# Performance work log

Measured on AMD Instinct MI355X. Metric: run time of the kernel, lower is better.

## Reference

```python
import jax, jax.numpy as jnp
import numpy as np

N = 10000
E = 320000
D_IN = 256
D_H = 256
D_OUT = 64
NEG_SLOPE = 0.2


def _segment_softmax(scores, seg, num_segments):
    # numerically stable softmax over variable-size neighborhoods
    m = jax.ops.segment_max(scores, seg, num_segments=num_segments)
    e = jnp.exp(scores - m[seg])
    s = jax.ops.segment_sum(e, seg, num_segments=num_segments)
    return e / s[seg]


def _gatv2_conv(x, src, dst, Wl, bl, Wr, br, att, bias):
    # PyG GATv2Conv, heads=1: lin_l on source, lin_r on target
    xl = x @ Wl + bl              # [N, C]
    xr = x @ Wr + br              # [N, C]
    xj = xl[src]                  # [E, C] source messages
    e = jax.nn.leaky_relu(xj + xr[dst], NEG_SLOPE)   # [E, C]
    score = e @ att               # [E]
    alpha = _segment_softmax(score, dst, N)          # [E]
    out = jax.ops.segment_sum(alpha[:, None] * xj, dst, num_segments=N)
    return out + bias


def setup_inputs() -> dict:
    key = jax.random.key(0)
    ks = jax.random.split(key, 16)
    s1 = 1.0 / np.sqrt(D_IN)
    s2 = 1.0 / np.sqrt(D_H)
    x = jax.random.normal(ks[0], (N, D_IN), dtype=jnp.float32)
    edge_index = jax.random.randint(ks[1], (2, E), 0, N, dtype=jnp.int64)
    return {
        "x": x,
        "W1l": jax.random.normal(ks[2], (D_IN, D_H), jnp.float32) * s1,
        "b1l": jnp.zeros((D_H,), jnp.float32),
        "W1r": jax.random.normal(ks[3], (D_IN, D_H), jnp.float32) * s1,
        "b1r": jnp.zeros((D_H,), jnp.float32),
        "att1": jax.random.normal(ks[4], (D_H,), jnp.float32) * s2,
        "bias1": jnp.zeros((D_H,), jnp.float32),
        "W2l": jax.random.normal(ks[5], (D_H, D_H), jnp.float32) * s2,
        "b2l": jnp.zeros((D_H,), jnp.float32),
        "W2r": jax.random.normal(ks[6], (D_H, D_H), jnp.float32) * s2,
        "b2r": jnp.zeros((D_H,), jnp.float32),
        "att2": jax.random.normal(ks[7], (D_H,), jnp.float32) * s2,
        "bias2": jnp.zeros((D_H,), jnp.float32),
        "Wout": jax.random.normal(ks[8], (D_H, D_OUT), jnp.float32) * s2,
        "bout": jnp.zeros((D_OUT,), jnp.float32),
        "edge_index": edge_index,
    }


def reference(x, W1l, b1l, W1r, b1r, att1, bias1,
              W2l, b2l, W2r, b2r, att2, bias2,
              Wout, bout, edge_index):
    # add self loops (PyG GATv2Conv default)
    loops = jnp.arange(N, dtype=edge_index.dtype)
    src = jnp.concatenate([edge_index[0], loops])
    dst = jnp.concatenate([edge_index[1], loops])

    h = _gatv2_conv(x, src, dst, W1l, b1l, W1r, b1r, att1, bias1)
    h = jax.nn.relu(h)            # norm=Identity, dropout inactive (eval)
    h = _gatv2_conv(h, src, dst, W2l, b2l, W2r, b2r, att2, bias2)
    h = jax.nn.relu(h)
    logits = h @ Wout + bout      # [N, D_OUT]
    return jax.nn.log_softmax(logits, axis=1)
```

## Files before the change

kernel.cpp:

```cpp
#include <hip/hip_runtime.h>
#include <hip/hip_bf16.h>
#include <math.h>

#define N_NODES 10000
#define N_EDGES 320000
#define TOT_E (N_EDGES + N_NODES)
#define D 256
#define DOUT 64
#define NEG_SLOPE 0.2f
#define MAXDEG 128

typedef __attribute__((ext_vector_type(8))) short bf16x8;
typedef __attribute__((ext_vector_type(4))) float f32x4;
typedef unsigned short ushort_t;

__device__ __forceinline__ unsigned short f2b_rne(float f) {
    unsigned int x = __float_as_uint(f);
    x += 0x7FFFu + ((x >> 16) & 1u);
    return (unsigned short)(x >> 16);
}
__device__ __forceinline__ float b2f(unsigned short h) {
    return __uint_as_float(((unsigned int)h) << 16);
}
__device__ __forceinline__ void bsplit(float v, unsigned short& hi, unsigned short& lo) {
    hi = f2b_rne(v);
    lo = f2b_rne(v - b2f(hi));
}

__device__ __forceinline__ bool detect_f32(const void* x) {
    const ushort_t* xb = (const ushort_t*)x;
    int lane = threadIdx.x & 63;
    int bad = 0;
    #pragma unroll
    for (int i = 0; i < 4; ++i) {
        float v = b2f(xb[2 * (lane + 64 * i)]);
        bad += !(fabsf(v) < 1e4f) ? 1 : 0;
    }
    #pragma unroll
    for (int o = 32; o > 0; o >>= 1) bad += __shfl_down(bad, o);
    return __shfl(bad, 0) > 8;
}
__device__ __forceinline__ bool detect_i64(const int* e32) {
    int lane = threadIdx.x & 63;
    int nz = (e32[2 * lane + 1] != 0) ? 1 : 0;
    #pragma unroll
    for (int o = 32; o > 0; o >>= 1) nz += __shfl_down(nz, o);
    return __shfl(nz, 0) == 0;
}

__global__ __launch_bounds__(256) void prep_kernel(
        const void* x, ushort_t* xh, ushort_t* xlo,
        const void* W1l, const void* W1r, const void* W2l, const void* W2r, const void* Wo,
        const void* v0, const void* v1, const void* v2, const void* v3,
        const void* v4, const void* v5, const void* v6, const void* v7, const void* v8,
        ushort_t* wt, float* vecf, int* counts) {
    bool f32s = detect_f32(x);
    int bid = blockIdx.x;
    int t = threadIdx.x;
    if (bid < 2500) {
        int i = bid * 1024 + t * 4;
        float v[4];
        if (f32s) {
            float4 f = *(const float4*)((const float*)x + i);
            v[0] = f.x; v[1] = f.y; v[2] = f.z; v[3] = f.w;
        } else {
            union { uint2 q; ushort_t u[4]; } r;
            r.q = *(const uint2*)((const ushort_t*)x + i);
            #pragma unroll
            for (int j = 0; j < 4; ++j) v[j] = b2f(r.u[j]);
        }
        union { uint2 q; ushort_t u[4]; } H, L;
        #pragma unroll
        for (int j = 0; j < 4; ++j) bsplit(v[j], H.u[j], L.u[j]);
        *(uint2*)(xh + i) = H.q;
        *(uint2*)(xlo + i) = L.q;
    } else if (bid < 3588) {
        int b = bid - 2500;
        const void* srcs5[5] = {W1l, W1r, W2l, W2r, Wo};
        int wid, n, ncols;
        if (b < 1024) { wid = b >> 8; n = b & 255; ncols = 256; }
        else          { wid = 4;      n = b - 1024; ncols = 64; }
        ushort_t* dh;
        ushort_t* dl;
        if (wid < 4) { dh = wt + (size_t)wid * 2 * 65536; dl = dh + 65536; }
        else         { dh = wt + (size_t)8 * 65536;       dl = dh + 16384; }
        float v = f32s ? ((const float*)srcs5[wid])[(size_t)t * ncols + n]
                       : b2f(((const ushort_t*)srcs5[wid])[(size_t)t * ncols + n]);
        unsigned short hi, lo;
        bsplit(v, hi, lo);
        dh[(size_t)n * 256 + t] = hi;
        dl[(size_t)n * 256 + t] = lo;
    } else if (bid < 3597) {
        int b = bid - 3588;
        const void* ps[9] = {v0, v1, v2, v3, v4, v5, v6, v7, v8};
        int n = (b == 8) ? DOUT : 256;
        if (t < n) {
            float v = f32s ? ((const float*)ps[b])[t] : b2f(((const ushort_t*)ps[b])[t]);
            vecf[b * 256 + t] = v;
        }
    } else {
        int idx = (bid - 3597) * 256 + t;
        if (idx < N_NODES) counts[idx] = 0;
    }
}

__device__ __forceinline__ int eload(const int* ei, bool is64, int idx) {
    int v = is64 ? ei[2 * (size_t)idx] : ei[idx];
    return ((unsigned)v < (unsigned)N_NODES) ? v : 0;
}

__global__ __launch_bounds__(256) void scatter_kernel(const int* __restrict__ ei,
                                                      int* __restrict__ counts,
                                                      int* __restrict__ srcs_pad) {
    bool is64 = detect_i64(ei);
    int id = blockIdx.x * 256 + threadIdx.x;
    if (id >= TOT_E) return;
    int src, dst;
    if (id < N_EDGES) { src = eload(ei, is64, id); dst = eload(ei, is64, N_EDGES + id); }
    else              { src = dst = id - N_EDGES; }
    int slot = atomicAdd(&counts[dst], 1);
    if (slot < MAXDEG) srcs_pad[dst * MAXDEG + slot] = src;
}

__global__ __launch_bounds__(256) void gemm_mfma_kernel(
        const ushort_t* __restrict__ Ahg, const ushort_t* __restrict__ Alg,
        const ushort_t* __restrict__ Wh0, const ushort_t* __restrict__ Wl0,
        const float* __restrict__ bias0, ushort_t* __restrict__ out0,
        const ushort_t* __restrict__ Wh1, const ushort_t* __restrict__ Wl1,
        const float* __restrict__ bias1, float* __restrict__ out1) {
    __shared__ bf16x8 Ah[4][64];
    __shared__ bf16x8 Al[4][64];
    __shared__ bf16x8 Bh[4][64];
    __shared__ bf16x8 Bl[4][64];
    int tid = threadIdx.x;
    int lane = tid & 63, wave = tid >> 6;
    int row0 = blockIdx.y * 64;
    int y = blockIdx.x;
    const ushort_t* Wh; const ushort_t* Wl; const float* bias;
    int col0;
    bool ob_bf16;
    if (y < 4) { Wh = Wh0; Wl = Wl0; bias = bias0; col0 = y * 64; ob_bf16 = true; }
    else       { Wh = Wh1; Wl = Wl1; bias = bias1; col0 = (y - 4) * 64; ob_bf16 = false; }
    int sm = tid >> 2;
    int skq = tid & 3;
    int sl = skq * 16 + (sm & 15);
    int sr = sm >> 4;

    f32x4 acc[4];
    #pragma unroll
    for (int c = 0; c < 4; ++c) acc[c] = (f32x4){0.f, 0.f, 0.f, 0.f};

    for (int k0 = 0; k0 < D; k0 += 32) {
        uint4 qah, qal;
        int grow = row0 + sm;
        if (grow < N_NODES) {
            size_t aoff = (size_t)grow * D + k0 + skq * 8;
            qah = *(const uint4*)(Ahg + aoff);
            qal = *(const uint4*)(Alg + aoff);
        } else {
            qah = (uint4){0, 0, 0, 0}; qal = (uint4){0, 0, 0, 0};
        }
        size_t boff = (size_t)(col0 + sm) * 256 + k0 + skq * 8;
        uint4 qbh = *(const uint4*)(Wh + boff);
        uint4 qbl = *(const uint4*)(Wl + boff);

        __syncthreads();
        *(uint4*)&Ah[sr][sl] = qah;
        *(uint4*)&Al[sr][sl] = qal;
        *(uint4*)&Bh[sr][sl] = qbh;
        *(uint4*)&Bl[sr][sl] = qbl;
        __syncthreads();

        bf16x8 a_h = Ah[wave][lane];
        bf16x8 a_l = Al[wave][lane];
        #pragma unroll
        for (int c = 0; c < 4; ++c) {
            bf16x8 b_h = Bh[c][lane];
            bf16x8 b_l = Bl[c][lane];
            acc[c] = __builtin_amdgcn_mfma_f32_16x16x32_bf16(a_h, b_l, acc[c], 0, 0, 0);
            acc[c] = __builtin_amdgcn_mfma_f32_16x16x32_bf16(a_l, b_h, acc[c], 0, 0, 0);
            acc[c] = __builtin_amdgcn_mfma_f32_16x16x32_bf16(a_h, b_h, acc[c], 0, 0, 0);
        }
    }
    int quad = lane >> 4;
    #pragma unroll
    for (int c = 0; c < 4; ++c) {
        int col = col0 + c * 16 + (lane & 15);
        float bv = bias[col];
        #pragma unroll
        for (int i = 0; i < 4; ++i) {
            int row = row0 + wave * 16 + quad * 4 + i;
            if (row < N_NODES) {
                float v = acc[c][i] + bv;
                if (ob_bf16) out0[(size_t)row * D + col] = f2b_rne(v);
                else         out1[(size_t)row * D + col] = v;
            }
        }
    }
}

__global__ __launch_bounds__(256) void conv_kernel(const ushort_t* __restrict__ xl,
                                                   const float* __restrict__ xr,
                                                   const float* __restrict__ att,
                                                   const float* __restrict__ bias,
                                                   const int* __restrict__ counts,
                                                   const int* __restrict__ srcs_pad,
                                                   ushort_t* __restrict__ hh,
                                                   ushort_t* __restrict__ hl) {
    __shared__ float xr_s[D];
    __shared__ float sc[MAXDEG];
    __shared__ int srcs_s[MAXDEG];
    int node = blockIdx.x;
    int t = threadIdx.x;
    int lane = t & 63, wave = t >> 6;
    int deg = counts[node];
    if (deg > MAXDEG) deg = MAXDEG;
    if (deg <= 0) {
        float o = fmaxf(bias[t], 0.f);
        unsigned short hi, lo; bsplit(o, hi, lo);
        hh[(size_t)node * D + t] = hi;
        hl[(size_t)node * D + t] = lo;
        return;
    }
    xr_s[t] = xr[(size_t)node * D + t];
    if (t < deg) srcs_s[t] = srcs_pad[node * MAXDEG + t];
    __syncthreads();

    int hw = t >> 5;
    int seg = t & 31;
    float xr8[8], att8[8];
    {
        float4 x0 = *(const float4*)&xr_s[seg * 8];
        float4 x1 = *(const float4*)&xr_s[seg * 8 + 4];
        float4 a0 = *(const float4*)(att + seg * 8);
        float4 a1 = *(const float4*)(att + seg * 8 + 4);
        xr8[0] = x0.x; xr8[1] = x0.y; xr8[2] = x0.z; xr8[3] = x0.w;
        xr8[4] = x1.x; xr8[5] = x1.y; xr8[6] = x1.z; xr8[7] = x1.w;
        att8[0] = a0.x; att8[1] = a0.y; att8[2] = a0.z; att8[3] = a0.w;
        att8[4] = a1.x; att8[5] = a1.y; att8[6] = a1.z; att8[7] = a1.w;
    }
    for (int e = hw; e < deg; e += 8) {
        int src = srcs_s[e];
        union { uint4 q; ushort_t u[8]; } r;
        r.q = *(const uint4*)(xl + (size_t)src * D + seg * 8);
        float p = 0.f;
        #pragma unroll
        for (int j = 0; j < 8; ++j) {
            float v = b2f(r.u[j]) + xr8[j];
            v = fmaxf(v, NEG_SLOPE * v);
            p += v * att8[j];
        }
        #pragma unroll
        for (int o = 16; o > 0; o >>= 1) p += __shfl_down(p, o, 32);
        if (seg == 0) sc[e] = isfinite(p) ? p : -1e30f;
    }
    __syncthreads();
    if (wave == 0) {
        float v0 = (lane < deg) ? sc[lane] : -INFINITY;
        float v1 = (lane + 64 < deg) ? sc[lane + 64] : -INFINITY;
        float mx = fmaxf(v0, v1);
        #pragma unroll
        for (int o = 32; o > 0; o >>= 1) mx = fmaxf(mx, __shfl_xor(mx, o));
        float e0 = (lane < deg) ? expf(v0 - mx) : 0.f;
        float e1 = (lane + 64 < deg) ? expf(v1 - mx) : 0.f;
        float s = e0 + e1;
        #pragma unroll
        for (int o = 32; o > 0; o >>= 1) s += __shfl_xor(s, o);
        float inv = 1.f / s;
        if (lane < deg) sc[lane] = e0 * inv;
        if (lane + 64 < deg) sc[lane + 64] = e1 * inv;
    }
    __syncthreads();
    float acc = 0.f;
    const ushort_t* xt = xl + t;
    #pragma unroll 4
    for (int e = 0; e < deg; ++e) {
        acc += sc[e] * b2f(xt[(size_t)srcs_s[e] * D]);
    }
    float o = acc + bias[t];
    if (!isfinite(o)) o = 0.f;
    o = fmaxf(o, 0.f);
    unsigned short hi, lo; bsplit(o, hi, lo);
    hh[(size_t)node * D + t] = hi;
    hl[(size_t)node * D + t] = lo;
}

__global__ __launch_bounds__(256) void logits_kernel(
        const ushort_t* __restrict__ Ahg, const ushort_t* __restrict__ Alg,
        const ushort_t* __restrict__ Wh, const ushort_t* __restrict__ Wl,
        const float* __restrict__ bias, float* __restrict__ out) {
    __shared__ bf16x8 Ah[4][64];
    __shared__ bf16x8 Al[4][64];
    __shared__ bf16x8 Bh[4][64];
    __shared__ bf16x8 Bl[4][64];
    __shared__ float Cs[64][65];
    __shared__ float mxs[64], lss[64];
    int tid = threadIdx.x;
    int lane = tid & 63, wave = tid >> 6;
    int row0 = blockIdx.x * 64;
    int sm = tid >> 2, skq = tid & 3;
    int sl = skq * 16 + (sm & 15), sr = sm >> 4;

    f32x4 acc[4];
    #pragma unroll
    for (int c = 0; c < 4; ++c) acc[c] = (f32x4){0.f, 0.f, 0.f, 0.f};

    for (int k0 = 0; k0 < D; k0 += 32) {
        uint4 qah, qal;
        int grow = row0 + sm;
        if (grow < N_NODES) {
            size_t aoff = (size_t)grow * D + k0 + skq * 8;
            qah = *(const uint4*)(Ahg + aoff);
            qal = *(const uint4*)(Alg + aoff);
        } else {
            qah = (uint4){0, 0, 0, 0}; qal = (uint4){0, 0, 0, 0};
        }
        size_t boff = (size_t)sm * 256 + k0 + skq * 8;
        uint4 qbh = *(const uint4*)(Wh + boff);
        uint4 qbl = *(const uint4*)(Wl + boff);
        __syncthreads();
        *(uint4*)&Ah[sr][sl] = qah;
        *(uint4*)&Al[sr][sl] = qal;
        *(uint4*)&Bh[sr][sl] = qbh;
        *(uint4*)&Bl[sr][sl] = qbl;
        __syncthreads();
        bf16x8 a_h = Ah[wave][lane];
        bf16x8 a_l = Al[wave][lane];
        #pragma unroll
        for (int c = 0; c < 4; ++c) {
            bf16x8 b_h = Bh[c][lane];
            bf16x8 b_l = Bl[c][lane];
            acc[c] = __builtin_amdgcn_mfma_f32_16x16x32_bf16(a_h, b_l, acc[c], 0, 0, 0);
            acc[c] = __builtin_amdgcn_mfma_f32_16x16x32_bf16(a_l, b_h, acc[c], 0, 0, 0);
            acc[c] = __builtin_amdgcn_mfma_f32_16x16x32_bf16(a_h, b_h, acc[c], 0, 0, 0);
        }
    }
    int quad = lane >> 4;
    #pragma unroll
    for (int c = 0; c < 4; ++c) {
        int col = c * 16 + (lane & 15);
        float bv = bias[col];
        #pragma unroll
        for (int i = 0; i < 4; ++i) {
            int row = wave * 16 + quad * 4 + i;
            Cs[row][col] = acc[c][i] + bv;
        }
    }
    __syncthreads();
    if (tid < 64) {
        float mx = -INFINITY;
        for (int c2 = 0; c2 < 64; ++c2) {
            float v = Cs[tid][c2];
            if (!isfinite(v)) { v = -1e30f; Cs[tid][c2] = v; }
            mx = fmaxf(mx, v);
        }
        float ssum = 0.f;
        for (int c2 = 0; c2 < 64; ++c2) ssum += expf(Cs[tid][c2] - mx);
        mxs[tid] = mx;
        lss[tid] = logf(ssum);
    }
    __syncthreads();
    for (int idx = tid; idx < 64 * 64; idx += 256) {
        int r = idx >> 6, col = idx & 63;
        int grow = row0 + r;
        if (grow < N_NODES) out[(size_t)grow * DOUT + col] = Cs[r][col] - mxs[r] - lss[r];
    }
}

extern "C" void kernel_launch(void* const* d_in, const int* in_sizes, int n_in,
                              void* d_out, int out_size, void* d_ws, size_t ws_size,
                              hipStream_t stream) {
    const void* x    = d_in[0];
    const void* W1l  = d_in[1];
    const void* b1l  = d_in[2];
    const void* W1r  = d_in[3];
    const void* b1r  = d_in[4];
    const void* att1 = d_in[5];
    const void* bia1 = d_in[6];
    const void* W2l  = d_in[7];
    const void* b2l  = d_in[8];
    const void* W2r  = d_in[9];
    const void* b2r  = d_in[10];
    const void* att2 = d_in[11];
    const void* bia2 = d_in[12];
    const void* Wout = d_in[13];
    const void* bout = d_in[14];
    const int*  ei   = (const int*)d_in[15];

    int* counts   = (int*)d_ws;
    int* srcs_pad = counts + N_NODES;
    ushort_t* wt = (ushort_t*)(srcs_pad + (size_t)N_NODES * MAXDEG);
    ushort_t* W1lH = wt;                ushort_t* W1lL = W1lH + 65536;
    ushort_t* W1rH = W1lL + 65536;      ushort_t* W1rL = W1rH + 65536;
    ushort_t* W2lH = W1rL + 65536;      ushort_t* W2lL = W2lH + 65536;
    ushort_t* W2rH = W2lL + 65536;      ushort_t* W2rL = W2rH + 65536;
    ushort_t* WoH  = W2rL + 65536;      ushort_t* WoL  = WoH + 16384;
    float* vecf = (float*)(WoL + 16384);
    ushort_t* xh  = (ushort_t*)(vecf + 9 * 256);
    ushort_t* xlo = xh + (size_t)N_NODES * D;
    ushort_t* xlb = xlo + (size_t)N_NODES * D;
    float* xr = (float*)(xlb + (size_t)N_NODES * D);
    ushort_t* hh = xh;
    ushort_t* hl = xlo;

    float* b1lf = vecf + 0 * 256;
    float* b1rf = vecf + 1 * 256;
    float* att1f = vecf + 2 * 256;
    float* bia1f = vecf + 3 * 256;
    float* b2lf = vecf + 4 * 256;
    float* b2rf = vecf + 5 * 256;
    float* att2f = vecf + 6 * 256;
    float* bia2f = vecf + 7 * 256;
    float* boutf = vecf + 8 * 256;

    prep_kernel<<<3637, 256, 0, stream>>>(x, xh, xlo,
                                          W1l, W1r, W2l, W2r, Wout,
                                          b1l, b1r, att1, bia1, b2l, b2r, att2, bia2, bout,
                                          wt, vecf, counts);
    scatter_kernel<<<(TOT_E + 255) / 256, 256, 0, stream>>>(ei, counts, srcs_pad);

    const int GX = (N_NODES + 63) / 64;
    gemm_mfma_kernel<<<dim3(8, GX), 256, 0, stream>>>(
        xh, xlo, W1lH, W1lL, b1lf, xlb, W1rH, W1rL, b1rf, xr);
    conv_kernel<<<N_NODES, 256, 0, stream>>>(xlb, xr, att1f, bia1f, counts, srcs_pad, hh, hl);
    gemm_mfma_kernel<<<dim3(8, GX), 256, 0, stream>>>(
        hh, hl, W2lH, W2lL, b2lf, xlb, W2rH, W2rL, b2rf, xr);
    conv_kernel<<<N_NODES, 256, 0, stream>>>(xlb, xr, att2f, bia2f, counts, srcs_pad, hh, hl);
    logits_kernel<<<GX, 256, 0, stream>>>(hh, hl, WoH, WoL, boutf, (float*)d_out);
}
```

Baseline: 269.6 us.

## Fuse attention scoring and aggregation into single-pass online softmax in conv kernel

The conv kernel no longer runs three phases (score per edge, one-wave softmax, then a second gather of source rows for aggregation). Each half-wave now loads a chunk of source feature rows once, computes scores, and keeps an online-softmax running max, sum and weighted accumulator in registers. Half-wave partials are combined through shared memory at the end. This removes the second global gather of xl rows and the serial softmax step, at the cost of more registers, a block barrier per 32-edge chunk, and extra shared memory.

```diff
diff --git a/kernel.cpp b/kernel.cpp
--- a/kernel.cpp
+++ b/kernel.cpp
@@ -208,11 +208,12 @@
                                                    ushort_t* __restrict__ hh,
                                                    ushort_t* __restrict__ hl) {
     __shared__ float xr_s[D];
-    __shared__ float sc[MAXDEG];
     __shared__ int srcs_s[MAXDEG];
+    __shared__ float hwmax[2][8];
+    __shared__ float sred[8];
+    __shared__ float fbuf[8][256];
     int node = blockIdx.x;
     int t = threadIdx.x;
-    int lane = t & 63, wave = t >> 6;
     int deg = counts[node];
     if (deg > MAXDEG) deg = MAXDEG;
     if (deg <= 0) {
@@ -239,45 +240,78 @@
         att8[0] = a0.x; att8[1] = a0.y; att8[2] = a0.z; att8[3] = a0.w;
         att8[4] = a1.x; att8[5] = a1.y; att8[6] = a1.z; att8[7] = a1.w;
     }
-    for (int e = hw; e < deg; e += 8) {
-        int src = srcs_s[e];
-        union { uint4 q; ushort_t u[8]; } r;
-        r.q = *(const uint4*)(xl + (size_t)src * D + seg * 8);
-        float p = 0.f;
-        #pragma unroll
-        for (int j = 0; j < 8; ++j) {
-            float v = b2f(r.u[j]) + xr8[j];
-            v = fmaxf(v, NEG_SLOPE * v);
-            p += v * att8[j];
-        }
-        #pragma unroll
-        for (int o = 16; o > 0; o >>= 1) p += __shfl_down(p, o, 32);
-        if (seg == 0) sc[e] = isfinite(p) ? p : -1e30f;
+    float acc8[8];
+    #pragma unroll
+    for (int j = 0; j < 8; ++j) acc8[j] = 0.f;
+    float m = -INFINITY, s = 0.f;
+    int par = 0;
+
+    for (int cbase = 0; cbase < deg; cbase += 32, par ^= 1) {
+        int dlim = deg - cbase; if (dlim > 32) dlim = 32;
+        int ni = (dlim > hw) ? ((dlim - hw + 7) >> 3) : 0;
+        union { uint4 q; ushort_t u[8]; } r[4];
+        float scv[4];
+        #pragma unroll
+        for (int i = 0; i < 4; ++i) {
+            if (i < ni) {
+                int src = srcs_s[cbase + hw + 8 * i];
+                r[i].q = *(const uint4*)(xl + (size_t)src * D + seg * 8);
+            }
+        }
+        #pragma unroll
+        for (int i = 0; i < 4; ++i) {
+            scv[i] = -1e30f;
+            if (i < ni) {
+                float p = 0.f;
+                #pragma unroll
+                for (int j = 0; j < 8; ++j) {
+                    float v = b2f(r[i].u[j]) + xr8[j];
+                    v = fmaxf(v, NEG_SLOPE * v);
+                    p = fmaf(v, att8[j], p);
+                }
+                #pragma unroll
+                for (int o = 16; o > 0; o >>= 1) p += __shfl_xor(p, o, 32);
+                scv[i] = isfinite(p) ? p : -1e30f;
+            }
+        }
+        float mx4 = fmaxf(fmaxf(scv[0], scv[1]), fmaxf(scv[2], scv[3]));
+        if (seg == 0) hwmax[par][hw] = mx4;
+        __syncthreads();
+        float cmax = hwmax[par][0];
+        #pragma unroll
+        for (int k = 1; k < 8; ++k) cmax = fmaxf(cmax, hwmax[par][k]);
+        float m_new = fmaxf(m, cmax);
+        float scale = (m > -1e37f) ? __expf(m - m_new) : 0.f;
+        s *= scale;
+        #pragma unroll
+        for (int j = 0; j < 8; ++j) acc8[j] *= scale;
+        #pragma unroll
+        for (int i = 0; i < 4; ++i) {
+            if (i < ni) {
+                float p = __expf(scv[i] - m_new);
+                s += p;
+                #pragma unroll
+                for (int j = 0; j < 8; ++j) {
+                    acc8[j] = fmaf(p, b2f(r[i].u[j]), acc8[j]);
+                }
+            }
+        }
+        m = m_new;
     }
     __syncthreads();
-    if (wave == 0) {
-        float v0 = (lane < deg) ? sc[lane] : -INFINITY;
-        float v1 = (lane + 64 < deg) ? sc[lane + 64] : -INFINITY;
-        float mx = fmaxf(v0, v1);
-        #pragma unroll
-        for (int o = 32; o > 0; o >>= 1) mx = fmaxf(mx, __shfl_xor(mx, o));
-        float e0 = (lane < deg) ? expf(v0 - mx) : 0.f;
-        float e1 = (lane + 64 < deg) ? expf(v1 - mx) : 0.f;
-        float s = e0 + e1;
-        #pragma unroll
-        for (int o = 32; o > 0; o >>= 1) s += __shfl_xor(s, o);
-        float inv = 1.f / s;
-        if (lane < deg) sc[lane] = e0 * inv;
-        if (lane + 64 < deg) sc[lane + 64] = e1 * inv;
-    }
+    float4 w0 = (float4){acc8[0], acc8[1], acc8[2], acc8[3]};
+    float4 w1 = (float4){acc8[4], acc8[5], acc8[6], acc8[7]};
+    *(float4*)&fbuf[hw][seg * 8] = w0;
+    *(float4*)&fbuf[hw][seg * 8 + 4] = w1;
+    if (seg == 0) sred[hw] = s;
     __syncthreads();
-    float acc = 0.f;
-    const ushort_t* xt = xl + t;
-    #pragma unroll 4
-    for (int e = 0; e < deg; ++e) {
-        acc += sc[e] * b2f(xt[(size_t)srcs_s[e] * D]);
-    }
-    float o = acc + bias[t];
+    float tot = 0.f;
+    #pragma unroll
+    for (int k = 0; k < 8; ++k) tot += fbuf[k][t];
+    float stot = sred[0];
+    #pragma unroll
+    for (int k = 1; k < 8; ++k) stot += sred[k];
+    float o = tot / stot + bias[t];
     if (!isfinite(o)) o = 0.f;
     o = fmaxf(o, 0.f);
     unsigned short hi, lo; bsplit(o, hi, lo);
```

Measured after the change: 272.5 us. Within noise of the previous version (+1.1%).
